# Kernel tuning notes

Measured on AMD Instinct MI355X. Metric: run time of the kernel, lower is better.

## Reference

```python
import jax, jax.numpy as jnp
import numpy as np

jax.config.update("jax_enable_x64", True)  # torch code upcasts to double inside generalized_mean

B, C, K = 32768, 1000, 10


def setup_inputs() -> dict:
    key = jax.random.key(0)
    k1, k2 = jax.random.split(key)
    y_pred = jax.random.normal(k1, (B, C), dtype=jnp.float32)
    # K distinct, sorted class indices per row (matches torch scatter/nonzero assumption)
    u = jax.random.uniform(k2, (B, C))
    y_attack = jnp.sort(jnp.argsort(u, axis=1)[:, :K], axis=1).astype(jnp.int32)
    return {"y_pred": y_pred, "y_attack": y_attack}


def _generalized_mean(x, p):
    # torch: cast to double, x**p, mean, **(1/p), cast back to original dtype
    x_type = x.dtype
    xd = x.astype(jnp.float64)
    return (jnp.mean(xd ** p, axis=-1) ** (1.0 / p)).astype(x_type)


def reference(y_pred, y_attack):
    CC = 5.0  # surjection constant c=5
    probs = jax.nn.softmax(y_pred, axis=-1)                      # [B, C]
    in_att = jnp.take_along_axis(probs, y_attack, axis=1)        # [B, K]
    # mask of attack classes; max over complement == torch gather-on-nonzero then max
    rows = jnp.arange(probs.shape[0])[:, None]
    mask = jnp.zeros(probs.shape, dtype=bool).at[rows, y_attack].set(True)
    not_in_attack_max = jnp.max(jnp.where(mask, -jnp.inf, probs), axis=-1)  # [B]
    in_attack_min = jnp.min(in_att, axis=-1)                                 # [B]
    macro_loss = not_in_attack_max - in_attack_min                           # [B]

    sorting = jnp.diff(in_att, axis=-1)                          # [B, K-1], in [-1, 1]
    sorting = CC + CC * sorting                                  # surject_to_positive
    sorting = _generalized_mean(sorting, 9.0)                    # p = self.p = 9
    sorting = (sorting - CC) / CC                                # surject_from_positive

    catted = jnp.stack([macro_loss, sorting], axis=-1)           # [B, 2]
    catted_pos = CC + CC * catted
    final_pos = _generalized_mean(catted_pos, 10.0)              # p = 10
    return (final_pos - CC) / CC                                 # [B]
```

## Files before the change

### kernel.cpp

```cpp
#include <hip/hip_runtime.h>
#include <math.h>


#define NC 1000
#define NK 10
#define NV4 250
#define L2E 1.44269504088896340736f

__global__ __launch_bounds__(256) void boiler_loss_kernel(
    const float* __restrict__ y_pred,
    const int*   __restrict__ y_att,
    float*       __restrict__ out,
    int B)
{
    const int wave = threadIdx.x >> 6;
    const int lane = threadIdx.x & 63;
    const int row  = blockIdx.x * 4 + wave;
    if (row >= B) return;

    const float* __restrict__ xrow = y_pred + (size_t)row * NC;
    const int*   __restrict__ arow = y_att + (size_t)row * NK;

    int aidx = (lane < NK) ? arow[lane] : 0;
    int att[NK];
    #pragma unroll
    for (int j = 0; j < NK; ++j) att[j] = __shfl(aidx, j, 64);

    const float aval = xrow[aidx];

    float v[16];
    const float4* __restrict__ xv = (const float4*)xrow;
    #pragma unroll
    for (int k = 0; k < 4; ++k) {
        const int i4 = lane + 64 * k;
        float4 f;
        if (i4 < NV4) f = xv[i4];
        else f = make_float4(-INFINITY, -INFINITY, -INFINITY, -INFINITY);
        v[4*k+0] = f.x; v[4*k+1] = f.y; v[4*k+2] = f.z; v[4*k+3] = f.w;
    }

    unsigned bits = 0u;
    #pragma unroll
    for (int j = 0; j < NK; ++j) {
        const int i4a   = att[j] >> 2;
        const int owner = i4a & 63;
        const int reg   = ((i4a >> 6) << 2) | (att[j] & 3);
        bits |= (owner == lane) ? (1u << reg) : 0u;
    }

    float mAll = -INFINITY, mNA = -INFINITY;
    #pragma unroll
    for (int r = 0; r < 16; ++r) {
        const float f = v[r];
        mAll = fmaxf(mAll, f);
        const float g = ((bits >> r) & 1u) ? -INFINITY : f;
        mNA = fmaxf(mNA, g);
    }
    #pragma unroll
    for (int off = 32; off > 0; off >>= 1) {
        mAll = fmaxf(mAll, __shfl_xor(mAll, off, 64));
        mNA  = fmaxf(mNA,  __shfl_xor(mNA,  off, 64));
    }

    const float mscale = -mAll * L2E;
    float s = 0.0f;
    #pragma unroll
    for (int r = 0; r < 16; ++r) s += exp2f(fmaf(v[r], L2E, mscale));
    #pragma unroll
    for (int off = 32; off > 0; off >>= 1) s += __shfl_xor(s, off, 64);

    const float rs = 1.0f / s;

    const float pjl = exp2f(fmaf(aval, L2E, mscale)) * rs;
    float p[NK];
    #pragma unroll
    for (int j = 0; j < NK; ++j) p[j] = __shfl(pjl, j, 64);

    if (lane == 0) {
        const float pNA = exp2f(fmaf(mNA, L2E, mscale)) * rs;
        float pmin = p[0];
        #pragma unroll
        for (int j = 1; j < NK; ++j) pmin = fminf(pmin, p[j]);
        const float macro_loss = pNA - pmin;

        float acc9 = 0.0f;
        #pragma unroll
        for (int j = 0; j < NK - 1; ++j) {
            const float sv = fmaf(5.0f, p[j+1] - p[j], 5.0f);
            const float x2 = sv * sv;
            const float x4 = x2 * x2;
            const float x8 = x4 * x4;
            acc9 = fmaf(x8, sv, acc9);
        }
        const float gm9 = exp2f(log2f(acc9 * (1.0f / 9.0f)) * (1.0f / 9.0f));
        const float sorting = (gm9 - 5.0f) * 0.2f;

        const float c0 = fmaf(5.0f, macro_loss, 5.0f);
        const float c1 = fmaf(5.0f, sorting, 5.0f);
        const float a2 = c0 * c0, a4 = a2 * a2, a8 = a4 * a4;
        const float b2 = c1 * c1, b4 = b2 * b2, b8 = b4 * b4;
        const float m10 = (a8 * a2 + b8 * b2) * 0.5f;
        const float gm10 = exp2f(log2f(m10) * 0.1f);

        out[row] = (gm10 - 5.0f) * 0.2f;
    }
}

extern "C" void kernel_launch(void* const* d_in, const int* in_sizes, int n_in,
                              void* d_out, int out_size, void* d_ws, size_t ws_size,
                              hipStream_t stream) {
    const float* y_pred = (const float*)d_in[0];
    const int*   y_att  = (const int*)d_in[1];
    float* out = (float*)d_out;
    const int B = in_sizes[0] / NC;
    const int blocks = (B + 3) / 4;
    boiler_loss_kernel<<<blocks, 256, 0, stream>>>(y_pred, y_att, out, B);
}
```

Measured before the change: 183.9 us.

## Skip masked max when row max is not an attack class; use native exp/log/rcp

Each row now gets the max over attack-class logits with a wave reduction. When that max is below the row max, the non-attack max equals the row max and its probability is just 1/sum, so the masked-max pass is skipped and only runs on a rare slow path. The per-row tail math is spread across lanes with shuffles instead of running serially on lane 0, and exp2, log2 and reciprocal use the raw AMDGCN builtins. This cuts ALU and shuffle work in a memory-bound kernel, at the cost of slightly lower precision in the transcendentals.

```diff
diff --git a/kernel.cpp b/kernel.cpp
--- a/kernel.cpp
+++ b/kernel.cpp
@@ -6,6 +6,22 @@
 #define NK 10
 #define NV4 250
 #define L2E 1.44269504088896340736f
+
+#if __has_builtin(__builtin_amdgcn_exp2f)
+#define EXP2F(x) __builtin_amdgcn_exp2f(x)
+#else
+#define EXP2F(x) exp2f(x)
+#endif
+#if __has_builtin(__builtin_amdgcn_logf)
+#define LOG2F(x) __builtin_amdgcn_logf(x)
+#else
+#define LOG2F(x) log2f(x)
+#endif
+#if __has_builtin(__builtin_amdgcn_rcpf)
+#define RCPF(x) __builtin_amdgcn_rcpf(x)
+#else
+#define RCPF(x) (1.0f / (x))
+#endif
 
 __global__ __launch_bounds__(256) void boiler_loss_kernel(
     const float* __restrict__ y_pred,
@@ -21,11 +37,7 @@
     const float* __restrict__ xrow = y_pred + (size_t)row * NC;
     const int*   __restrict__ arow = y_att + (size_t)row * NK;
 
-    int aidx = (lane < NK) ? arow[lane] : 0;
-    int att[NK];
-    #pragma unroll
-    for (int j = 0; j < NK; ++j) att[j] = __shfl(aidx, j, 64);
-
+    const int aidx = arow[lane < NK ? lane : (NK - 1)];
     const float aval = xrow[aidx];
 
     float v[16];
@@ -39,68 +51,79 @@
         v[4*k+0] = f.x; v[4*k+1] = f.y; v[4*k+2] = f.z; v[4*k+3] = f.w;
     }
 
-    unsigned bits = 0u;
-    #pragma unroll
-    for (int j = 0; j < NK; ++j) {
-        const int i4a   = att[j] >> 2;
-        const int owner = i4a & 63;
-        const int reg   = ((i4a >> 6) << 2) | (att[j] & 3);
-        bits |= (owner == lane) ? (1u << reg) : 0u;
-    }
-
-    float mAll = -INFINITY, mNA = -INFINITY;
-    #pragma unroll
-    for (int r = 0; r < 16; ++r) {
-        const float f = v[r];
-        mAll = fmaxf(mAll, f);
-        const float g = ((bits >> r) & 1u) ? -INFINITY : f;
-        mNA = fmaxf(mNA, g);
-    }
+    float mAll = fmaxf(fmaxf(fmaxf(v[0], v[1]), fmaxf(v[2], v[3])),
+                       fmaxf(fmaxf(v[4], v[5]), fmaxf(v[6], v[7])));
+    mAll = fmaxf(mAll,
+                 fmaxf(fmaxf(fmaxf(v[8], v[9]), fmaxf(v[10], v[11])),
+                       fmaxf(fmaxf(v[12], v[13]), fmaxf(v[14], v[15]))));
+    float mAtt = aval;
     #pragma unroll
     for (int off = 32; off > 0; off >>= 1) {
         mAll = fmaxf(mAll, __shfl_xor(mAll, off, 64));
-        mNA  = fmaxf(mNA,  __shfl_xor(mNA,  off, 64));
+        mAtt = fmaxf(mAtt, __shfl_xor(mAtt, off, 64));
     }
 
     const float mscale = -mAll * L2E;
     float s = 0.0f;
     #pragma unroll
-    for (int r = 0; r < 16; ++r) s += exp2f(fmaf(v[r], L2E, mscale));
+    for (int r = 0; r < 16; ++r) s += EXP2F(fmaf(v[r], L2E, mscale));
     #pragma unroll
     for (int off = 32; off > 0; off >>= 1) s += __shfl_xor(s, off, 64);
 
-    const float rs = 1.0f / s;
+    const float rs = RCPF(s);
 
-    const float pjl = exp2f(fmaf(aval, L2E, mscale)) * rs;
-    float p[NK];
+    float pNA;
+    if (mAtt < mAll) {
+        pNA = rs;
+    } else {
+        unsigned bits = 0u;
+        #pragma unroll
+        for (int j = 0; j < NK; ++j) {
+            const int aj    = arow[j];
+            const int i4a   = aj >> 2;
+            const int owner = i4a & 63;
+            const int reg   = ((i4a >> 6) << 2) | (aj & 3);
+            bits |= (owner == lane) ? (1u << reg) : 0u;
+        }
+        float mNA = -INFINITY;
+        #pragma unroll
+        for (int r = 0; r < 16; ++r)
+            mNA = fmaxf(mNA, ((bits >> r) & 1u) ? -INFINITY : v[r]);
+        #pragma unroll
+        for (int off = 32; off > 0; off >>= 1)
+            mNA = fmaxf(mNA, __shfl_xor(mNA, off, 64));
+        pNA = EXP2F(fmaf(mNA, L2E, mscale)) * rs;
+    }
+
+    const float pj = EXP2F(fmaf(aval, L2E, mscale)) * rs;
+
+    float pmin = pj;
+    const float pnext = __shfl_down(pj, 1, 64);
+    float t9;
+    {
+        const float sv = fmaf(5.0f, pnext - pj, 5.0f);
+        const float x2 = sv * sv;
+        const float x4 = x2 * x2;
+        const float x8 = x4 * x4;
+        t9 = (lane < NK - 1) ? x8 * sv : 0.0f;
+    }
     #pragma unroll
-    for (int j = 0; j < NK; ++j) p[j] = __shfl(pjl, j, 64);
+    for (int off = 8; off > 0; off >>= 1) {
+        pmin = fminf(pmin, __shfl_xor(pmin, off, 64));
+        t9  += __shfl_xor(t9, off, 64);
+    }
 
     if (lane == 0) {
-        const float pNA = exp2f(fmaf(mNA, L2E, mscale)) * rs;
-        float pmin = p[0];
-        #pragma unroll
-        for (int j = 1; j < NK; ++j) pmin = fminf(pmin, p[j]);
+        const float gm9 = EXP2F(LOG2F(t9 * (1.0f / 9.0f)) * (1.0f / 9.0f));
+        const float sorting = (gm9 - 5.0f) * 0.2f;
         const float macro_loss = pNA - pmin;
-
-        float acc9 = 0.0f;
-        #pragma unroll
-        for (int j = 0; j < NK - 1; ++j) {
-            const float sv = fmaf(5.0f, p[j+1] - p[j], 5.0f);
-            const float x2 = sv * sv;
-            const float x4 = x2 * x2;
-            const float x8 = x4 * x4;
-            acc9 = fmaf(x8, sv, acc9);
-        }
-        const float gm9 = exp2f(log2f(acc9 * (1.0f / 9.0f)) * (1.0f / 9.0f));
-        const float sorting = (gm9 - 5.0f) * 0.2f;
 
         const float c0 = fmaf(5.0f, macro_loss, 5.0f);
         const float c1 = fmaf(5.0f, sorting, 5.0f);
         const float a2 = c0 * c0, a4 = a2 * a2, a8 = a4 * a4;
         const float b2 = c1 * c1, b4 = b2 * b2, b8 = b4 * b4;
         const float m10 = (a8 * a2 + b8 * b2) * 0.5f;
-        const float gm10 = exp2f(log2f(m10) * 0.1f);
+        const float gm10 = EXP2F(LOG2F(m10) * 0.1f);
 
         out[row] = (gm10 - 5.0f) * 0.2f;
     }
```

Result: no change. 183.9 us (-0.0%).
